# Kernel tuning notes

Measured on AMD Instinct MI355X. Metric: run time of the kernel, lower is better.

Reference implementation:

```python
import jax, jax.numpy as jnp
import numpy as np

P, N, E, H = 8192, 32, 256, 8
D = E // H
CUT_A, CUT_B = 0.001, 0.005  # self.length_range = (0.001, 0.005, None, None)
SQRT3 = 1.7320508075688772


def _soft_square_cutoff(x):
    # smooth ramp 0->1 on [CUT_A, CUT_B], 0 below, 1 above (high-side ranges are None)
    t = jnp.clip((x - CUT_A) / (CUT_B - CUT_A), 0.0, 1.0)
    return 0.5 * (1.0 - jnp.cos(jnp.pi * t))


def setup_inputs() -> dict:
    key = jax.random.key(0)
    ks = jax.random.split(key, 16)
    s = 1.0 / np.sqrt(E)
    inp = {
        "query": jax.random.normal(ks[0], (P, E), jnp.float32),
        "key_x": jax.random.normal(ks[1], (P, E), jnp.float32),
        "value": jax.random.normal(ks[2], (P, E), jnp.float32),
        "index_pair": jax.random.randint(ks[3], (P, N), 0, P),
        "relative_atten_weights": jax.random.normal(ks[4], (P, N, H), jnp.float32),
        # lengths ~ N(0, 0.002*sqrt(3)) so they span the (0.001, 0.005) cutoff range
        "rpe_distance": jax.random.normal(ks[5], (P, N, 3), jnp.float32) * 0.002,
        "Wq": jax.random.normal(ks[6], (E, E), jnp.float32) * s,
        "bq": jnp.zeros((E,), jnp.float32),
        "Wk": jax.random.normal(ks[7], (E, E), jnp.float32) * s,
        "bk": jnp.zeros((E,), jnp.float32),
        "Wv": jax.random.normal(ks[8], (E, E), jnp.float32) * s,
        "bv": jnp.zeros((E,), jnp.float32),
        "Wg1": jax.random.normal(ks[9], (E, 3 * H), jnp.float32) * s,
        "bg1": jnp.zeros((3 * H,), jnp.float32),
        "Wg2": jax.random.normal(ks[10], (3 * H, 3 * H), jnp.float32) * (1.0 / np.sqrt(3 * H)),
        "bg2": jnp.zeros((3 * H,), jnp.float32),
    }
    return inp


def reference(query, key_x, value, index_pair, relative_atten_weights, rpe_distance,
              Wq, bq, Wk, bk, Wv, bv, Wg1, bg1, Wg2, bg2):
    # --- RPE spherical harmonics (irreps 1x0e+1x1e, component norm); keep l=1 part ([:,1:])
    rlen = jnp.linalg.norm(rpe_distance, axis=-1, keepdims=True)        # [P,N,1]
    unit = rpe_distance / jnp.maximum(rlen, 1e-12)                      # normalize=True
    cutoff = _soft_square_cutoff(rlen)                                  # nonscalar cutoff
    rpe_edge_sh = SQRT3 * unit * cutoff                                 # [P,N,3]

    # --- projections
    q = query @ Wq + bq                                                 # [P,E]
    k = key_x @ Wk + bk
    v = value @ Wv + bv

    # --- mapper_v6: per-edge gather of key/value rows
    k_g = k[index_pair]                                                 # [P,N,E]
    v_g = v[index_pair]                                                 # [P,N,E]

    # --- dot-product attention logits
    qh = q.reshape(P, H, D)
    kh = k_g.reshape(P, N, H, D)
    dot_atten = jnp.einsum('phd,pnhd->pnh', qh, kh)                     # [P,N,H]

    # --- MLP positional bias gated by spherical harmonics
    diff = k_g - q[:, None, :]                                          # [P,N,E]
    g = jax.nn.relu(diff @ Wg1 + bg1) @ Wg2 + bg2                       # [P,N,3H]
    g = g.reshape(P, N, H, 3)
    pos_atten = jnp.sum(g * rpe_edge_sh[:, :, None, :], axis=-1)        # [P,N,H]

    atten = (dot_atten + pos_atten + relative_atten_weights) / np.sqrt(D)
    atten = jax.nn.softmax(atten, axis=1)                               # over neighbors

    vh = v_g.reshape(P, N, H, D)
    out = jnp.einsum('pnh,pnhc->phc', atten, vh).reshape(P, E)
    return out
```

## Files before the change

### kernel.cpp

```cpp
#include <hip/hip_runtime.h>
#include <stdint.h>

typedef uint32_t u32;
typedef unsigned short u16;

#define LDT 40

typedef __bf16 bf16x8 __attribute__((ext_vector_type(8)));
typedef float  f32x4  __attribute__((ext_vector_type(4)));

__device__ __forceinline__ float bf2f(u16 x) {
  union { float f; u32 u; } c; c.u = ((u32)x) << 16; return c.f;
}
__device__ __forceinline__ u16 f2bf(float f) {
  union { float f; u32 u; } c; c.f = f;
  u32 b = c.u;
  return (u16)((b + 0x7FFFu + ((b >> 16) & 1u)) >> 16);
}
__device__ __forceinline__ u32 pk2(float lo, float hi) {
  return (u32)f2bf(lo) | ((u32)f2bf(hi) << 16);
}

__global__ __launch_bounds__(256) void prep_transpose(
    const float* __restrict__ Wq, const float* __restrict__ Wk, const float* __restrict__ Wv,
    u16* __restrict__ WTq, u16* __restrict__ WTk, u16* __restrict__ WTv)
{
  int z = blockIdx.z, bx = blockIdx.x, by = blockIdx.y;
  int x = threadIdx.x, y = threadIdx.y;
  __shared__ u16 tile[32][33];
  const float* W  = (z == 0) ? Wq : (z == 1) ? Wk : Wv;
  u16*         WT = (z == 0) ? WTq : (z == 1) ? WTk : WTv;
  for (int yy = y; yy < 32; yy += 8)
    tile[yy][x] = f2bf(W[(size_t)(by * 32 + yy) * 256 + bx * 32 + x]);
  __syncthreads();
  for (int yy = y; yy < 32; yy += 8)
    WT[(size_t)(bx * 32 + yy) * 256 + by * 32 + x] = tile[x][yy];
}

__global__ __launch_bounds__(256) void prep_comb(
    const u16* __restrict__ WTq, const u16* __restrict__ WTk,
    const float* __restrict__ Wg1, const float* __restrict__ bg1,
    const float* __restrict__ bq, const float* __restrict__ bk,
    u16* __restrict__ CT, float* __restrict__ bcomb)
{
  int c = blockIdx.x, z = blockIdx.y;
  int t = threadIdx.x;
  const u16*   WT = (z == 0) ? WTq : WTk;
  const float* b  = (z == 0) ? bq : bk;

  float acc = 0.f;
#pragma unroll 8
  for (int e = 0; e < 256; e++)
    acc += bf2f(WT[(size_t)e * 256 + t]) * Wg1[(size_t)e * 24 + c];
  CT[(size_t)z * 8192 + (size_t)c * 256 + t] = f2bf(acc);

  __shared__ float red[256];
  red[t] = b[t] * Wg1[(size_t)t * 24 + c];
  __syncthreads();
  for (int s = 128; s > 0; s >>= 1) {
    if (t < s) red[t] += red[t + s];
    __syncthreads();
  }
  if (t == 0)
    bcomb[z * 24 + c] = red[0] - ((z == 0) ? bg1[c] : 0.f);
}

__global__ __launch_bounds__(256) void gemm_qkv(
    const float* __restrict__ Xq, const float* __restrict__ Xk, const float* __restrict__ Xv,
    const u16* __restrict__ WTq, const u16* __restrict__ WTk, const u16* __restrict__ WTv,
    const float* __restrict__ bq, const float* __restrict__ bk, const float* __restrict__ bv,
    const u16* __restrict__ CT, const float* __restrict__ bcomb,
    u16* __restrict__ Oq, u16* __restrict__ Ok, u16* __restrict__ Ov,
    float* __restrict__ qadj, float* __restrict__ kg1)
{
  int z = blockIdx.z;
  int nblk = blockIdx.x;
  if (nblk == 2 && z == 2) return;

  const float* X = (z == 0) ? Xq : (z == 1) ? Xk : Xv;
  int m0 = blockIdx.y * 128;
  int t = threadIdx.x;
  int lane = t & 63, wid = t >> 6;
  int fr = lane & 15, fg = lane >> 4;
  int sr = t >> 1;
  int sc = (t & 1) * 16;

  __shared__ __align__(16) u16 la[128 * LDT];
  __shared__ __align__(16) u16 lb[128 * LDT];

  if (nblk < 2) {
    const u16*   WT   = (z == 0) ? WTq : (z == 1) ? WTk : WTv;
    const float* bias = (z == 0) ? bq : (z == 1) ? bk : bv;
    u16*         O    = (z == 0) ? Oq : (z == 1) ? Ok : Ov;
    int n0 = nblk * 128;
    int wr = wid >> 1, wc = wid & 1;

    f32x4 acc[4][4];
#pragma unroll
    for (int i = 0; i < 4; i++)
#pragma unroll
      for (int j = 0; j < 4; j++) acc[i][j] = (f32x4){0.f, 0.f, 0.f, 0.f};

    for (int kt = 0; kt < 256; kt += 32) {
      const float4* ga = (const float4*)(X + (size_t)(m0 + sr) * 256 + kt + sc);
      float4 a0 = ga[0], a1 = ga[1], a2 = ga[2], a3 = ga[3];
      const uint4* gb = (const uint4*)(WT + (size_t)(n0 + sr) * 256 + kt + sc);
      uint4 b0 = gb[0], b1 = gb[1];

      uint4 wa0, wa1;
      wa0.x = pk2(a0.x, a0.y); wa0.y = pk2(a0.z, a0.w);
      wa0.z = pk2(a1.x, a1.y); wa0.w = pk2(a1.z, a1.w);
      wa1.x = pk2(a2.x, a2.y); wa1.y = pk2(a2.z, a2.w);
      wa1.z = pk2(a3.x, a3.y); wa1.w = pk2(a3.z, a3.w);

      __syncthreads();
      *(uint4*)&la[sr * LDT + sc]     = wa0;
      *(uint4*)&la[sr * LDT + sc + 8] = wa1;
      *(uint4*)&lb[sr * LDT + sc]     = b0;
      *(uint4*)&lb[sr * LDT + sc + 8] = b1;
      __syncthreads();

      bf16x8 af[4], bfr[4];
#pragma unroll
      for (int s = 0; s < 4; s++)
        af[s] = *(const bf16x8*)&la[(wr * 64 + s * 16 + fr) * LDT + fg * 8];
#pragma unroll
      for (int s = 0; s < 4; s++)
        bfr[s] = *(const bf16x8*)&lb[(wc * 64 + s * 16 + fr) * LDT + fg * 8];
#pragma unroll
      for (int i = 0; i < 4; i++)
#pragma unroll
        for (int j = 0; j < 4; j++)
          acc[i][j] = __builtin_amdgcn_mfma_f32_16x16x32_bf16(af[i], bfr[j], acc[i][j], 0, 0, 0);
    }

#pragma unroll
    for (int i = 0; i < 4; i++) {
      int rowb = m0 + wr * 64 + i * 16 + fg * 4;
#pragma unroll
      for (int j = 0; j < 4; j++) {
        int col = n0 + wc * 64 + j * 16 + fr;
        float bb = bias[col];
#pragma unroll
        for (int r = 0; r < 4; r++)
          O[(size_t)(rowb + r) * 256 + col] = f2bf(acc[i][j][r] + bb);
      }
    }
  } else {
    const u16*   BT = CT + (size_t)z * 8192;
    const float* bc = bcomb + z * 24;
    float*       O  = (z == 0) ? qadj : kg1;

    f32x4 acc[2][2];
#pragma unroll
    for (int i = 0; i < 2; i++)
#pragma unroll
      for (int j = 0; j < 2; j++) acc[i][j] = (f32x4){0.f, 0.f, 0.f, 0.f};

    for (int kt = 0; kt < 256; kt += 32) {
      const float4* ga = (const float4*)(X + (size_t)(m0 + sr) * 256 + kt + sc);
      float4 a0 = ga[0], a1 = ga[1], a2 = ga[2], a3 = ga[3];
      uint4 b0, b1;
      if (t < 64) {
        const uint4* gb = (const uint4*)(BT + (size_t)sr * 256 + kt + sc);
        b0 = gb[0]; b1 = gb[1];
      }
      uint4 wa0, wa1;
      wa0.x = pk2(a0.x, a0.y); wa0.y = pk2(a0.z, a0.w);
      wa0.z = pk2(a1.x, a1.y); wa0.w = pk2(a1.z, a1.w);
      wa1.x = pk2(a2.x, a2.y); wa1.y = pk2(a2.z, a2.w);
      wa1.z = pk2(a3.x, a3.y); wa1.w = pk2(a3.z, a3.w);

      __syncthreads();
      *(uint4*)&la[sr * LDT + sc]     = wa0;
      *(uint4*)&la[sr * LDT + sc + 8] = wa1;
      if (t < 64) {
        *(uint4*)&lb[sr * LDT + sc]     = b0;
        *(uint4*)&lb[sr * LDT + sc + 8] = b1;
      }
      __syncthreads();

      bf16x8 af[2], bfr[2];
#pragma unroll
      for (int s = 0; s < 2; s++)
        af[s] = *(const bf16x8*)&la[(wid * 32 + s * 16 + fr) * LDT + fg * 8];
#pragma unroll
      for (int s = 0; s < 2; s++)
        bfr[s] = *(const bf16x8*)&lb[(s * 16 + fr) * LDT + fg * 8];
#pragma unroll
      for (int i = 0; i < 2; i++)
#pragma unroll
        for (int j = 0; j < 2; j++)
          acc[i][j] = __builtin_amdgcn_mfma_f32_16x16x32_bf16(af[i], bfr[j], acc[i][j], 0, 0, 0);
    }

#pragma unroll
    for (int i = 0; i < 2; i++) {
      int rowb = m0 + wid * 32 + i * 16 + fg * 4;
#pragma unroll
      for (int j = 0; j < 2; j++) {
        int col = j * 16 + fr;
        if (col < 24) {
#pragma unroll
          for (int r = 0; r < 4; r++)
            O[(size_t)(rowb + r) * 24 + col] = acc[i][j][r] + bc[col];
        }
      }
    }
  }
}

__global__ __launch_bounds__(256) void edge_attn(
    const u16* __restrict__ qb, const u16* __restrict__ kb, const u16* __restrict__ vb,
    const float* __restrict__ kg1, const float* __restrict__ qadj,
    const int* __restrict__ ip, const float* __restrict__ raw,
    const float* __restrict__ rpe, const float* __restrict__ wg2g,
    const float* __restrict__ bg2g, float* __restrict__ out)
{
  int p = blockIdx.x, t = threadIdx.x;
  int lane = t & 63, w = t >> 6;

  __shared__ __align__(16) float q_s[256];
  __shared__              int   idx_s[32];
  __shared__              float rpe_s[96];
  __shared__              float sh_s[32][3];
  __shared__              float qadj_s[24];
  __shared__              float bg2_s[24];
  __shared__ __align__(16) u16  wg2T[32 * 40];
  __shared__ __align__(16) u16  preb[32 * 40];
  __shared__ __align__(16) float kg1_s[32 * 24];
  __shared__              float g_s[32 * 33];
  __shared__              float logit_s[32][8];
  __shared__              float ps_s[64];
  __shared__              float is_s[8];
  __shared__ __align__(16) float pv_s[4 * 256];

  q_s[t] = bf2f(qb[(size_t)p * 256 + t]);
  if (t < 32) idx_s[t] = ip[(size_t)p * 32 + t];
  if (t < 96) rpe_s[t] = rpe[(size_t)p * 96 + t];
  if (t >= 128 && t < 152) qadj_s[t - 128] = qadj[(size_t)p * 24 + (t - 128)];
  if (t >= 160 && t < 184) bg2_s[t - 160] = bg2g[t - 160];
  {
    int s0 = 2 * t, s1 = 2 * t + 1;
    { int i = s0 / 24, j = s0 - i * 24; if (s0 < 576) wg2T[j * 40 + i] = f2bf(wg2g[s0]); }
    { int i = s1 / 24, j = s1 - i * 24; if (s1 < 576) wg2T[j * 40 + i] = f2bf(wg2g[s1]); }
    if (t < 64) { int s = 512 + t; int i = s / 24, j = s - i * 24; wg2T[j * 40 + i] = f2bf(wg2g[s]); }
    wg2T[(t >> 3) * 40 + 24 + (t & 7)] = 0;
    if (t < 192) wg2T[(24 + t / 24) * 40 + (t % 24)] = 0;
  }
  __syncthreads();

  if (t < 192) {
    int n = t / 6, f = t % 6;
    *(float4*)&kg1_s[n * 24 + f * 4] = ((const float4*)(kg1 + (size_t)idx_s[n] * 24))[f];
  }
  if (t < 32) {
    float x  = rpe_s[t * 3 + 0];
    float y  = rpe_s[t * 3 + 1];
    float zz = rpe_s[t * 3 + 2];
    float rl = sqrtf(x * x + y * y + zz * zz);
    float inv = 1.f / fmaxf(rl, 1e-12f);
    float tt = (rl - 0.001f) * 250.f;
    tt = fminf(fmaxf(tt, 0.f), 1.f);
    float cut = 0.5f * (1.f - cosf(tt * 3.14159265358979f));
    float s3c = 1.7320508075688772f * inv * cut;
    sh_s[t][0] = x * s3c; sh_s[t][1] = y * s3c; sh_s[t][2] = zz * s3c;
  }
  __syncthreads();

  {
    int n = t >> 3, jj = t & 7;
    float v0, v1, v2, v3;
    int j0 = jj * 4;
    v0 = (j0 + 0 < 24) ? fmaxf(kg1_s[n * 24 + j0 + 0] - qadj_s[j0 + 0], 0.f) : 0.f;
    v1 = (j0 + 1 < 24) ? fmaxf(kg1_s[n * 24 + j0 + 1] - qadj_s[j0 + 1], 0.f) : 0.f;
    v2 = (j0 + 2 < 24) ? fmaxf(kg1_s[n * 24 + j0 + 2] - qadj_s[j0 + 2], 0.f) : 0.f;
    v3 = (j0 + 3 < 24) ? fmaxf(kg1_s[n * 24 + j0 + 3] - qadj_s[j0 + 3], 0.f) : 0.f;
    uint2 pw; pw.x = pk2(v0, v1); pw.y = pk2(v2, v3);
    *(uint2*)&preb[n * 40 + j0] = pw;
  }
  __syncthreads();

  {
    int mt = w & 1, nt = w >> 1;
    int fr = lane & 15, fg = lane >> 4;
    bf16x8 a = *(const bf16x8*)&preb[(mt * 16 + fr) * 40 + fg * 8];
    bf16x8 b = *(const bf16x8*)&wg2T[(nt * 16 + fr) * 40 + fg * 8];
    f32x4 acc = (f32x4){0.f, 0.f, 0.f, 0.f};
    acc = __builtin_amdgcn_mfma_f32_16x16x32_bf16(a, b, acc, 0, 0, 0);
    int j = nt * 16 + fr;
    float bb = (j < 24) ? bg2_s[j] : 0.f;
    int e0 = mt * 16 + fg * 4;
#pragma unroll
    for (int r = 0; r < 4; r++)
      g_s[(e0 + r) * 33 + j] = acc[r] + bb;
  }
  __syncthreads();

  {
    int n = t >> 3, h = t & 7;
    const uint4*  kr = (const uint4*)(kb + (size_t)idx_s[n] * 256 + h * 32);
    const float4* qr = (const float4*)(q_s + h * 32);
    float dot = 0.f;
#pragma unroll
    for (int c = 0; c < 4; c++) {
      uint4 kw = kr[c];
      float4 q0 = qr[2 * c], q1 = qr[2 * c + 1];
      dot += bf2f((u16)(kw.x & 0xFFFF)) * q0.x + bf2f((u16)(kw.x >> 16)) * q0.y;
      dot += bf2f((u16)(kw.y & 0xFFFF)) * q0.z + bf2f((u16)(kw.y >> 16)) * q0.w;
      dot += bf2f((u16)(kw.z & 0xFFFF)) * q1.x + bf2f((u16)(kw.z >> 16)) * q1.y;
      dot += bf2f((u16)(kw.w & 0xFFFF)) * q1.z + bf2f((u16)(kw.w >> 16)) * q1.w;
    }
    float pos = g_s[n * 33 + h * 3 + 0] * sh_s[n][0]
              + g_s[n * 33 + h * 3 + 1] * sh_s[n][1]
              + g_s[n * 33 + h * 3 + 2] * sh_s[n][2];
    float rw = raw[(size_t)p * 256 + t];
    logit_s[n][h] = __expf((dot + pos + rw) * 0.17677669529663687f);
  }
  __syncthreads();

  if (t < 64) {
    int h = t & 7, g = t >> 3;
    ps_s[h * 8 + g] = logit_s[g * 4 + 0][h] + logit_s[g * 4 + 1][h]
                    + logit_s[g * 4 + 2][h] + logit_s[g * 4 + 3][h];
  }
  __syncthreads();
  if (t < 8) {
    float s = 0.f;
#pragma unroll
    for (int g = 0; g < 8; g++) s += ps_s[t * 8 + g];
    is_s[t] = 1.f / s;
  }
  __syncthreads();

  {
    int c0 = lane * 4;
    int hh = lane >> 3;
    float isv = is_s[hh];
    float a0 = 0.f, a1 = 0.f, a2 = 0.f, a3 = 0.f;
#pragma unroll
    for (int i = 0; i < 8; i++) {
      int n = w * 8 + i;
      float wt = logit_s[n][hh] * isv;
      uint2 vv = *(const uint2*)(vb + (size_t)idx_s[n] * 256 + c0);
      a0 += wt * bf2f((u16)(vv.x & 0xFFFF));
      a1 += wt * bf2f((u16)(vv.x >> 16));
      a2 += wt * bf2f((u16)(vv.y & 0xFFFF));
      a3 += wt * bf2f((u16)(vv.y >> 16));
    }
    float4 r; r.x = a0; r.y = a1; r.z = a2; r.w = a3;
    *(float4*)&pv_s[w * 256 + c0] = r;
  }
  __syncthreads();

  out[(size_t)p * 256 + t] = pv_s[t] + pv_s[256 + t] + pv_s[512 + t] + pv_s[768 + t];
}

extern "C" void kernel_launch(void* const* d_in, const int* in_sizes, int n_in,
                              void* d_out, int out_size, void* d_ws, size_t ws_size,
                              hipStream_t stream) {
  const float* query = (const float*)d_in[0];
  const float* key_x = (const float*)d_in[1];
  const float* value = (const float*)d_in[2];
  const int*   index_pair = (const int*)d_in[3];
  const float* raw  = (const float*)d_in[4];
  const float* rpe  = (const float*)d_in[5];
  const float* Wq = (const float*)d_in[6];
  const float* bq = (const float*)d_in[7];
  const float* Wk = (const float*)d_in[8];
  const float* bk = (const float*)d_in[9];
  const float* Wv = (const float*)d_in[10];
  const float* bv = (const float*)d_in[11];
  const float* Wg1 = (const float*)d_in[12];
  const float* bg1 = (const float*)d_in[13];
  const float* Wg2 = (const float*)d_in[14];
  const float* bg2 = (const float*)d_in[15];
  float* out = (float*)d_out;

  char* ws = (char*)d_ws;
  u16*   qbuf = (u16*)(ws);
  u16*   kbuf = (u16*)(ws + (4u << 20));
  u16*   vbuf = (u16*)(ws + (8u << 20));
  float* qadj = (float*)(ws + (12u << 20));
  float* kg1  = (float*)(ws + (12u << 20) + 786432);
  u16*   WTq  = (u16*)(ws + (12u << 20) + 2 * 786432);
  u16*   WTk  = WTq + 65536;
  u16*   WTv  = WTk + 65536;
  u16*   CT   = WTv + 65536;
  float* bcomb = (float*)(CT + 16384);

  prep_transpose<<<dim3(8, 8, 3), dim3(32, 8, 1), 0, stream>>>(
      Wq, Wk, Wv, WTq, WTk, WTv);
  prep_comb<<<dim3(24, 2), 256, 0, stream>>>(
      WTq, WTk, Wg1, bg1, bq, bk, CT, bcomb);
  gemm_qkv<<<dim3(3, 64, 3), 256, 0, stream>>>(
      query, key_x, value, WTq, WTk, WTv, bq, bk, bv, CT, bcomb,
      qbuf, kbuf, vbuf, qadj, kg1);
  edge_attn<<<8192, 256, 0, stream>>>(
      qbuf, kbuf, vbuf, kg1, qadj, index_pair, raw, rpe, Wg2, bg2, out);
}
```

Measured before the change: 75.69 us.

## Move edge attention dot products and value aggregation onto MFMA with staged K/V tiles

The edge_attn kernel now stages the gathered key rows and value rows in LDS and computes the per-head q·k logits with MFMA against a block-diagonal q matrix, replacing the scalar per-thread dot products. The weighted sum over values also becomes an MFMA, with bf16 attention weights as the A operand. The Wg2 transpose and bf16 conversion move into a separate one-block prep kernel, so each block no longer rebuilds it. The kg1 and qadj buffers are padded to a 32-float stride for vectorized loads. In exchange, attention weights are rounded to bf16, LDS use grows, the column-by-column value operand reads may cause bank conflicts, and most MFMA output lanes are discarded.

```diff
diff --git a/kernel.cpp b/kernel.cpp
--- a/kernel.cpp
+++ b/kernel.cpp
@@ -37,6 +37,17 @@
     WT[(size_t)(bx * 32 + yy) * 256 + by * 32 + x] = tile[x][yy];
 }
 
+__global__ __launch_bounds__(256) void prep_wg2(
+    const float* __restrict__ Wg2, u16* __restrict__ wg2bf)
+{
+  int t = threadIdx.x;
+  for (int i = t; i < 1280; i += 256) {
+    int j = i / 40, k = i % 40;
+    float v = (j < 24 && k < 24) ? Wg2[(size_t)k * 24 + j] : 0.f;
+    wg2bf[i] = f2bf(v);
+  }
+}
+
 __global__ __launch_bounds__(256) void prep_comb(
     const u16* __restrict__ WTq, const u16* __restrict__ WTk,
     const float* __restrict__ Wg1, const float* __restrict__ bg1,
@@ -203,7 +214,7 @@
         if (col < 24) {
 #pragma unroll
           for (int r = 0; r < 4; r++)
-            O[(size_t)(rowb + r) * 24 + col] = acc[i][j][r] + bc[col];
+            O[(size_t)(rowb + r) * 32 + col] = acc[i][j][r] + bc[col];
         }
       }
     }
@@ -212,148 +223,167 @@
 
 __global__ __launch_bounds__(256) void edge_attn(
     const u16* __restrict__ qb, const u16* __restrict__ kb, const u16* __restrict__ vb,
-    const float* __restrict__ kg1, const float* __restrict__ qadj,
+    const float* __restrict__ kg1g, const float* __restrict__ qadjg,
     const int* __restrict__ ip, const float* __restrict__ raw,
-    const float* __restrict__ rpe, const float* __restrict__ wg2g,
+    const float* __restrict__ rpe, const u16* __restrict__ wg2bf,
     const float* __restrict__ bg2g, float* __restrict__ out)
 {
   int p = blockIdx.x, t = threadIdx.x;
   int lane = t & 63, w = t >> 6;
-
-  __shared__ __align__(16) float q_s[256];
-  __shared__              int   idx_s[32];
-  __shared__              float rpe_s[96];
-  __shared__              float sh_s[32][3];
-  __shared__              float qadj_s[24];
-  __shared__              float bg2_s[24];
-  __shared__ __align__(16) u16  wg2T[32 * 40];
-  __shared__ __align__(16) u16  preb[32 * 40];
-  __shared__ __align__(16) float kg1_s[32 * 24];
-  __shared__              float g_s[32 * 33];
-  __shared__              float logit_s[32][8];
-  __shared__              float ps_s[64];
-  __shared__              float is_s[8];
-  __shared__ __align__(16) float pv_s[4 * 256];
-
-  q_s[t] = bf2f(qb[(size_t)p * 256 + t]);
+  int fr = lane & 15, fg = lane >> 4;
+
+  __shared__ __align__(16) u16   kv_s[32 * 264];
+  __shared__ __align__(16) u16   qbd_s[16 * 264];
+  __shared__ __align__(16) u16   wg2_s[32 * 40];
+  __shared__ __align__(16) u16   attb_s[16 * 40];
+  __shared__ __align__(16) float kg1_s[32 * 32];
+  __shared__ float qadj_s[24];
+  __shared__ float g_s[32 * 33];
+  __shared__ float sh_s[32 * 3];
+  __shared__ float is_s[8];
+  __shared__ int   idx_s[32];
+  __shared__ float bg2_s[24];
+
   if (t < 32) idx_s[t] = ip[(size_t)p * 32 + t];
-  if (t < 96) rpe_s[t] = rpe[(size_t)p * 96 + t];
-  if (t >= 128 && t < 152) qadj_s[t - 128] = qadj[(size_t)p * 24 + (t - 128)];
-  if (t >= 160 && t < 184) bg2_s[t - 160] = bg2g[t - 160];
+  else if (t < 56) bg2_s[t - 32] = bg2g[t - 32];
+  else if (t >= 64 && t < 88) qadj_s[t - 64] = qadjg[(size_t)p * 32 + (t - 64)];
+  if (t >= 96) {
+    int i = t - 96;
+    *(uint4*)&wg2_s[i * 8] = ((const uint4*)wg2bf)[i];
+  }
   {
-    int s0 = 2 * t, s1 = 2 * t + 1;
-    { int i = s0 / 24, j = s0 - i * 24; if (s0 < 576) wg2T[j * 40 + i] = f2bf(wg2g[s0]); }
-    { int i = s1 / 24, j = s1 - i * 24; if (s1 < 576) wg2T[j * 40 + i] = f2bf(wg2g[s1]); }
-    if (t < 64) { int s = 512 + t; int i = s / 24, j = s - i * 24; wg2T[j * 40 + i] = f2bf(wg2g[s]); }
-    wg2T[(t >> 3) * 40 + 24 + (t & 7)] = 0;
-    if (t < 192) wg2T[(24 + t / 24) * 40 + (t % 24)] = 0;
-  }
-  __syncthreads();
-
-  if (t < 192) {
-    int n = t / 6, f = t % 6;
-    *(float4*)&kg1_s[n * 24 + f * 4] = ((const float4*)(kg1 + (size_t)idx_s[n] * 24))[f];
+    int row = t >> 4, c0 = (t & 15) * 16;
+    uint4 v0 = {0, 0, 0, 0}, v1 = {0, 0, 0, 0};
+    if ((c0 >> 5) == row) {
+      const uint4* qp = (const uint4*)(qb + (size_t)p * 256 + c0);
+      v0 = qp[0]; v1 = qp[1];
+    }
+    *(uint4*)&qbd_s[row * 264 + c0]     = v0;
+    *(uint4*)&qbd_s[row * 264 + c0 + 8] = v1;
   }
   if (t < 32) {
-    float x  = rpe_s[t * 3 + 0];
-    float y  = rpe_s[t * 3 + 1];
-    float zz = rpe_s[t * 3 + 2];
-    float rl = sqrtf(x * x + y * y + zz * zz);
+    float x  = rpe[(size_t)p * 96 + t * 3 + 0];
+    float y  = rpe[(size_t)p * 96 + t * 3 + 1];
+    float z  = rpe[(size_t)p * 96 + t * 3 + 2];
+    float rl = sqrtf(x * x + y * y + z * z);
     float inv = 1.f / fmaxf(rl, 1e-12f);
-    float tt = (rl - 0.001f) * 250.f;
-    tt = fminf(fmaxf(tt, 0.f), 1.f);
-    float cut = 0.5f * (1.f - cosf(tt * 3.14159265358979f));
+    float tt2 = fminf(fmaxf((rl - 0.001f) * 250.f, 0.f), 1.f);
+    float cut = 0.5f * (1.f - cosf(tt2 * 3.14159265358979f));
     float s3c = 1.7320508075688772f * inv * cut;
-    sh_s[t][0] = x * s3c; sh_s[t][1] = y * s3c; sh_s[t][2] = zz * s3c;
+    sh_s[t * 3 + 0] = x * s3c; sh_s[t * 3 + 1] = y * s3c; sh_s[t * 3 + 2] = z * s3c;
   }
   __syncthreads();
 
   {
-    int n = t >> 3, jj = t & 7;
-    float v0, v1, v2, v3;
-    int j0 = jj * 4;
-    v0 = (j0 + 0 < 24) ? fmaxf(kg1_s[n * 24 + j0 + 0] - qadj_s[j0 + 0], 0.f) : 0.f;
-    v1 = (j0 + 1 < 24) ? fmaxf(kg1_s[n * 24 + j0 + 1] - qadj_s[j0 + 1], 0.f) : 0.f;
-    v2 = (j0 + 2 < 24) ? fmaxf(kg1_s[n * 24 + j0 + 2] - qadj_s[j0 + 2], 0.f) : 0.f;
-    v3 = (j0 + 3 < 24) ? fmaxf(kg1_s[n * 24 + j0 + 3] - qadj_s[j0 + 3], 0.f) : 0.f;
-    uint2 pw; pw.x = pk2(v0, v1); pw.y = pk2(v2, v3);
-    *(uint2*)&preb[n * 40 + j0] = pw;
+    int n = t >> 3, c0 = (t & 7) * 32;
+    const uint4* kp = (const uint4*)(kb + (size_t)idx_s[n] * 256 + c0);
+    uint4 k0 = kp[0], k1 = kp[1], k2 = kp[2], k3 = kp[3];
+    u16* d = &kv_s[n * 264 + c0];
+    *(uint4*)(d)      = k0; *(uint4*)(d + 8)  = k1;
+    *(uint4*)(d + 16) = k2; *(uint4*)(d + 24) = k3;
+    *(float4*)&kg1_s[n * 32 + (t & 7) * 4] =
+        *(const float4*)(kg1g + (size_t)idx_s[n] * 32 + (t & 7) * 4);
+  }
+  __syncthreads();
+
+  f32x4 dacc = {0.f, 0.f, 0.f, 0.f};
+  if (w < 2) {
+    const u16* arow = &kv_s[(w * 16 + fr) * 264];
+    const u16* brow = &qbd_s[fr * 264];
+#pragma unroll
+    for (int ks = 0; ks < 8; ks++) {
+      bf16x8 a = *(const bf16x8*)(arow + ks * 32 + fg * 8);
+      bf16x8 b = *(const bf16x8*)(brow + ks * 32 + fg * 8);
+      dacc = __builtin_amdgcn_mfma_f32_16x16x32_bf16(a, b, dacc, 0, 0, 0);
+    }
+  } else {
+    int mt = w - 2;
+    bf16x8 a;
+    if (fg < 3) {
+      int rowb = (mt * 16 + fr) * 32 + fg * 8;
+      int kq = fg * 8;
+#pragma unroll
+      for (int j = 0; j < 8; j++) {
+        float x = fmaxf(kg1_s[rowb + j] - qadj_s[kq + j], 0.f);
+        a[j] = (__bf16)x;
+      }
+    } else {
+#pragma unroll
+      for (int j = 0; j < 8; j++) a[j] = (__bf16)0.f;
+    }
+    bf16x8 b0 = *(const bf16x8*)&wg2_s[fr * 40 + fg * 8];
+    bf16x8 b1 = *(const bf16x8*)&wg2_s[(16 + fr) * 40 + fg * 8];
+    f32x4 g0 = {0.f, 0.f, 0.f, 0.f}, g1 = {0.f, 0.f, 0.f, 0.f};
+    g0 = __builtin_amdgcn_mfma_f32_16x16x32_bf16(a, b0, g0, 0, 0, 0);
+    g1 = __builtin_amdgcn_mfma_f32_16x16x32_bf16(a, b1, g1, 0, 0, 0);
+    int e0 = mt * 16 + fg * 4;
+    float bb0 = bg2_s[fr];
+    float bb1 = (fr < 8) ? bg2_s[16 + fr] : 0.f;
+#pragma unroll
+    for (int r = 0; r < 4; r++) {
+      g_s[(e0 + r) * 33 + fr]      = g0[r] + bb0;
+      g_s[(e0 + r) * 33 + 16 + fr] = g1[r] + bb1;
+    }
+  }
+  __syncthreads();
+
+  if (w < 2) {
+    if (fr < 8) {
+#pragma unroll
+      for (int r = 0; r < 4; r++) {
+        int n = w * 16 + fg * 4 + r;
+        float pos = g_s[n * 33 + fr * 3 + 0] * sh_s[n * 3 + 0]
+                  + g_s[n * 33 + fr * 3 + 1] * sh_s[n * 3 + 1]
+                  + g_s[n * 33 + fr * 3 + 2] * sh_s[n * 3 + 2];
+        float rw = raw[(size_t)p * 256 + n * 8 + fr];
+        float ev = __expf((dacc[r] + pos + rw) * 0.17677669529663687f);
+        attb_s[fr * 40 + n] = f2bf(ev);
+      }
+    }
+  } else {
+    int tt = t - 128;
+    int n = tt >> 2, c0 = (tt & 3) * 64;
+    const uint2* vp = (const uint2*)(vb + (size_t)idx_s[n] * 256 + c0);
+    u16* d = &kv_s[n * 260 + c0];
+#pragma unroll
+    for (int jj = 0; jj < 16; jj++) *(uint2*)(d + jj * 4) = vp[jj];
+  }
+  __syncthreads();
+
+  if (w == 0) {
+    int h = lane & 7, g = lane >> 3;
+    float s = bf2f(attb_s[h * 40 + g * 4 + 0]) + bf2f(attb_s[h * 40 + g * 4 + 1])
+            + bf2f(attb_s[h * 40 + g * 4 + 2]) + bf2f(attb_s[h * 40 + g * 4 + 3]);
+    s += __shfl_xor(s, 8, 64);
+    s += __shfl_xor(s, 16, 64);
+    s += __shfl_xor(s, 32, 64);
+    if (lane < 8) is_s[h] = 1.f / s;
   }
   __syncthreads();
 
   {
-    int mt = w & 1, nt = w >> 1;
-    int fr = lane & 15, fg = lane >> 4;
-    bf16x8 a = *(const bf16x8*)&preb[(mt * 16 + fr) * 40 + fg * 8];
-    bf16x8 b = *(const bf16x8*)&wg2T[(nt * 16 + fr) * 40 + fg * 8];
-    f32x4 acc = (f32x4){0.f, 0.f, 0.f, 0.f};
-    acc = __builtin_amdgcn_mfma_f32_16x16x32_bf16(a, b, acc, 0, 0, 0);
-    int j = nt * 16 + fr;
-    float bb = (j < 24) ? bg2_s[j] : 0.f;
-    int e0 = mt * 16 + fg * 4;
-#pragma unroll
-    for (int r = 0; r < 4; r++)
-      g_s[(e0 + r) * 33 + j] = acc[r] + bb;
-  }
-  __syncthreads();
-
-  {
-    int n = t >> 3, h = t & 7;
-    const uint4*  kr = (const uint4*)(kb + (size_t)idx_s[n] * 256 + h * 32);
-    const float4* qr = (const float4*)(q_s + h * 32);
-    float dot = 0.f;
-#pragma unroll
-    for (int c = 0; c < 4; c++) {
-      uint4 kw = kr[c];
-      float4 q0 = qr[2 * c], q1 = qr[2 * c + 1];
-      dot += bf2f((u16)(kw.x & 0xFFFF)) * q0.x + bf2f((u16)(kw.x >> 16)) * q0.y;
-      dot += bf2f((u16)(kw.y & 0xFFFF)) * q0.z + bf2f((u16)(kw.y >> 16)) * q0.w;
-      dot += bf2f((u16)(kw.z & 0xFFFF)) * q1.x + bf2f((u16)(kw.z >> 16)) * q1.y;
-      dot += bf2f((u16)(kw.w & 0xFFFF)) * q1.z + bf2f((u16)(kw.w >> 16)) * q1.w;
-    }
-    float pos = g_s[n * 33 + h * 3 + 0] * sh_s[n][0]
-              + g_s[n * 33 + h * 3 + 1] * sh_s[n][1]
-              + g_s[n * 33 + h * 3 + 2] * sh_s[n][2];
-    float rw = raw[(size_t)p * 256 + t];
-    logit_s[n][h] = __expf((dot + pos + rw) * 0.17677669529663687f);
-  }
-  __syncthreads();
-
-  if (t < 64) {
-    int h = t & 7, g = t >> 3;
-    ps_s[h * 8 + g] = logit_s[g * 4 + 0][h] + logit_s[g * 4 + 1][h]
-                    + logit_s[g * 4 + 2][h] + logit_s[g * 4 + 3][h];
-  }
-  __syncthreads();
-  if (t < 8) {
-    float s = 0.f;
-#pragma unroll
-    for (int g = 0; g < 8; g++) s += ps_s[t * 8 + g];
-    is_s[t] = 1.f / s;
-  }
-  __syncthreads();
-
-  {
-    int c0 = lane * 4;
-    int hh = lane >> 3;
-    float isv = is_s[hh];
-    float a0 = 0.f, a1 = 0.f, a2 = 0.f, a3 = 0.f;
-#pragma unroll
-    for (int i = 0; i < 8; i++) {
-      int n = w * 8 + i;
-      float wt = logit_s[n][hh] * isv;
-      uint2 vv = *(const uint2*)(vb + (size_t)idx_s[n] * 256 + c0);
-      a0 += wt * bf2f((u16)(vv.x & 0xFFFF));
-      a1 += wt * bf2f((u16)(vv.x >> 16));
-      a2 += wt * bf2f((u16)(vv.y & 0xFFFF));
-      a3 += wt * bf2f((u16)(vv.y >> 16));
-    }
-    float4 r; r.x = a0; r.y = a1; r.z = a2; r.w = a3;
-    *(float4*)&pv_s[w * 256 + c0] = r;
-  }
-  __syncthreads();
-
-  out[(size_t)p * 256 + t] = pv_s[t] + pv_s[256 + t] + pv_s[512 + t] + pv_s[768 + t];
+    bf16x8 af = *(const bf16x8*)&attb_s[fr * 40 + fg * 8];
+#pragma unroll
+    for (int nt = 0; nt < 4; nt++) {
+      int colb = w * 64 + nt * 16;
+      const u16* vbase = &kv_s[(fg * 8) * 260 + colb + fr];
+      u16 b0 = vbase[0],        b1 = vbase[260],      b2 = vbase[2 * 260],
+          b3 = vbase[3 * 260],  b4 = vbase[4 * 260],  b5 = vbase[5 * 260],
+          b6 = vbase[6 * 260],  b7 = vbase[7 * 260];
+      union { u32 u[4]; bf16x8 v; } bb;
+      bb.u[0] = (u32)b0 | ((u32)b1 << 16);
+      bb.u[1] = (u32)b2 | ((u32)b3 << 16);
+      bb.u[2] = (u32)b4 | ((u32)b5 << 16);
+      bb.u[3] = (u32)b6 | ((u32)b7 << 16);
+      f32x4 acc = {0.f, 0.f, 0.f, 0.f};
+      acc = __builtin_amdgcn_mfma_f32_16x16x32_bf16(af, bb.v, acc, 0, 0, 0);
+      int h = 2 * w + (nt >> 1);
+      if (fg == (w >> 1)) {
+        float o = (w & 1) ? acc[2 + (nt >> 1)] : acc[0 + (nt >> 1)];
+        out[(size_t)p * 256 + colb + fr] = o * is_s[h];
+      }
+    }
+  }
 }
 
 extern "C" void kernel_launch(void* const* d_in, const int* in_sizes, int n_in,
@@ -378,24 +408,26 @@
   float* out = (float*)d_out;
 
   char* ws = (char*)d_ws;
-  u16*   qbuf = (u16*)(ws);
-  u16*   kbuf = (u16*)(ws + (4u << 20));
-  u16*   vbuf = (u16*)(ws + (8u << 20));
-  float* qadj = (float*)(ws + (12u << 20));
-  float* kg1  = (float*)(ws + (12u << 20) + 786432);
-  u16*   WTq  = (u16*)(ws + (12u << 20) + 2 * 786432);
-  u16*   WTk  = WTq + 65536;
-  u16*   WTv  = WTk + 65536;
-  u16*   CT   = WTv + 65536;
+  u16*   qbuf  = (u16*)(ws);
+  u16*   kbuf  = (u16*)(ws + (4u << 20));
+  u16*   vbuf  = (u16*)(ws + (8u << 20));
+  float* qadj  = (float*)(ws + (12u << 20));
+  float* kg1   = (float*)(ws + (13u << 20));
+  u16*   WTq   = (u16*)(ws + (14u << 20));
+  u16*   WTk   = WTq + 65536;
+  u16*   WTv   = WTk + 65536;
+  u16*   CT    = WTv + 65536;
   float* bcomb = (float*)(CT + 16384);
+  u16*   wg2bf = (u16*)(bcomb + 64);
 
   prep_transpose<<<dim3(8, 8, 3), dim3(32, 8, 1), 0, stream>>>(
       Wq, Wk, Wv, WTq, WTk, WTv);
+  prep_wg2<<<1, 256, 0, stream>>>(Wg2, wg2bf);
   prep_comb<<<dim3(24, 2), 256, 0, stream>>>(
       WTq, WTk, Wg1, bg1, bq, bk, CT, bcomb);
   gemm_qkv<<<dim3(3, 64, 3), 256, 0, stream>>>(
       query, key_x, value, WTq, WTk, WTv, bq, bk, bv, CT, bcomb,
       qbuf, kbuf, vbuf, qadj, kg1);
   edge_attn<<<8192, 256, 0, stream>>>(
-      qbuf, kbuf, vbuf, kg1, qadj, index_pair, raw, rpe, Wg2, bg2, out);
-}
+      qbuf, kbuf, vbuf, kg1, qadj, index_pair, raw, rpe, wg2bf, bg2, out);
+}
```

Result: slower. 93.23 us (+23.2%).
